# Kernel optimization log

Measured on AMD Instinct MI355X. Metric: run time of the kernel, lower is better.

The kernel has to match this reference:

```python
import math
import jax, jax.numpy as jnp
import numpy as np

B, S, D = 4, 2048, 1024
L = 2                      # codec_decoder_transformer_lengths entry
H, HD = 8, 128             # n_heads == n_kv_heads (no GQA repeat)
FF = 4096
WINDOW = 16                # sliding window (causal: keys in [i-16, i])
NORM_EPS = 0.01
QK_EPS = 1e-6
SCALE_INIT = 0.1           # layer_id < 18 -> 0.1


def _alibi_slopes(n):
    # n is a power of 2 here (8)
    r = 2.0 ** (-8.0 / n)
    return jnp.array([r ** (i + 1) for i in range(n)], dtype=jnp.float32)


def rms_norm(x, w, eps):
    return x * jax.lax.rsqrt(jnp.mean(x * x, axis=-1, keepdims=True) + eps) * w


def _attn_bias(dtype):
    pos = jnp.arange(S)
    rel = pos[None, :] - pos[:, None]          # [S,S], rel = j - i
    slopes = _alibi_slopes(H).astype(dtype)
    bias = slopes[:, None, None] * rel[None].astype(dtype)   # [H,S,S]
    mask = (rel > 0) | (rel < -WINDOW)         # causal + sliding window
    return jnp.where(mask[None], -jnp.inf, bias)


def setup_inputs() -> dict:
    key = jax.random.key(0)
    ks = jax.random.split(key, 9)
    sd = 0.02
    w = lambda k, shape: jax.random.normal(k, shape, jnp.float32) * sd
    return {
        "x": jax.random.normal(ks[0], (B, S, D), jnp.float32),
        "wq": w(ks[1], (L, D, H * HD)),
        "wk": w(ks[2], (L, D, H * HD)),
        "wv": w(ks[3], (L, D, H * HD)),
        "wo": w(ks[4], (L, H * HD, D)),
        "q_norm_w": jnp.ones((L, H * HD), jnp.float32),
        "k_norm_w": jnp.ones((L, H * HD), jnp.float32),
        "w1": w(ks[5], (L, D, FF)),
        "w2": w(ks[6], (L, FF, D)),
        "w3": w(ks[7], (L, D, FF)),
        "attn_norm_w": jnp.ones((L, D), jnp.float32),
        "ffn_norm_w": jnp.ones((L, D), jnp.float32),
        "attn_scale": jnp.full((L, D), SCALE_INIT, jnp.float32),
        "ffn_scale": jnp.full((L, D), SCALE_INIT, jnp.float32),
    }


def reference(x, wq, wk, wv, wo, q_norm_w, k_norm_w, w1, w2, w3,
              attn_norm_w, ffn_norm_w, attn_scale, ffn_scale):
    bias = _attn_bias(x.dtype)                 # [H,S,S]
    inv_sqrt_d = 1.0 / math.sqrt(HD)

    def block(h, p):
        (lwq, lwk, lwv, lwo, qnw, knw, lw1, lw2, lw3, anw, fnw, asc, fsc) = p
        xn = rms_norm(h, anw, NORM_EPS)
        # qk_norm applied on the flat (H*HD) projection before the head split
        q = rms_norm(xn @ lwq, qnw, QK_EPS).reshape(B, S, H, HD).transpose(0, 2, 1, 3)
        k = rms_norm(xn @ lwk, knw, QK_EPS).reshape(B, S, H, HD).transpose(0, 2, 1, 3)
        v = (xn @ lwv).reshape(B, S, H, HD).transpose(0, 2, 1, 3)
        scores = jnp.einsum('bhqd,bhkd->bhqk', q, k) * inv_sqrt_d + bias[None]
        attn = jax.nn.softmax(scores, axis=-1)
        y = jnp.einsum('bhqk,bhkd->bhqd', attn, v)
        y = y.transpose(0, 2, 1, 3).reshape(B, S, H * HD)
        h = h + asc * (y @ lwo)
        xn = rms_norm(h, fnw, NORM_EPS)
        ff = (jax.nn.silu(xn @ lw1) * (xn @ lw3)) @ lw2
        return h + fsc * ff, None

    out, _ = jax.lax.scan(
        block, x,
        (wq, wk, wv, wo, q_norm_w, k_norm_w, w1, w2, w3,
         attn_norm_w, ffn_norm_w, attn_scale, ffn_scale))
    return out
```

## Files before the change

### kernel.cpp

```cpp
#include <hip/hip_runtime.h>

#define B_ 4
#define S_ 2048
#define D_ 1024
#define H_ 8
#define HD_ 128
#define FF_ 4096
#define R_ (B_*S_)

typedef __attribute__((ext_vector_type(8))) short short8;
typedef __attribute__((ext_vector_type(4))) float f32x4;

__device__ __forceinline__ unsigned short f2bf(float f) {
  unsigned int u = __float_as_uint(f);
  return (unsigned short)((u + 0x7fffu + ((u >> 16) & 1u)) >> 16);
}
__device__ __forceinline__ float bf2f(unsigned short s) {
  return __uint_as_float(((unsigned int)s) << 16);
}

typedef const __attribute__((address_space(1))) unsigned int* gas_p;
typedef __attribute__((address_space(3))) unsigned int* las_p;
__device__ __forceinline__ void gload16(const void* g, void* l) {
  __builtin_amdgcn_global_load_lds((gas_p)g, (las_p)l, 16, 0, 0);
}

__global__ __launch_bounds__(256) void f2bf_t_all(
    const float* __restrict__ wq, const float* __restrict__ wk,
    const float* __restrict__ wv, const float* __restrict__ wo,
    const float* __restrict__ w1, const float* __restrict__ w3,
    const float* __restrict__ w2,
    unsigned short* __restrict__ qkvt, unsigned short* __restrict__ wot,
    unsigned short* __restrict__ w1t, unsigned short* __restrict__ w3t,
    unsigned short* __restrict__ w2t) {
  const int id = blockIdx.x;
  const int l = id >> 14, r = id & 16383;
  const float* src; unsigned short* dst; int Rows, Cols, t2;
  if (r < 4096) {
    Rows = 1024; Cols = 1024; t2 = r & 1023;
    const int wsel = r >> 10;
    if (wsel == 0)      { src = wq + (size_t)l*1048576u; dst = qkvt + (size_t)l*3145728u; }
    else if (wsel == 1) { src = wk + (size_t)l*1048576u; dst = qkvt + (size_t)l*3145728u + 1048576u; }
    else if (wsel == 2) { src = wv + (size_t)l*1048576u; dst = qkvt + (size_t)l*3145728u + 2097152u; }
    else                { src = wo + (size_t)l*1048576u; dst = wot + (size_t)l*1048576u; }
  } else if (r < 12288) {
    Rows = 1024; Cols = 4096; t2 = (r - 4096) & 4095;
    if (r < 8192) { src = w1 + (size_t)l*4194304u; dst = w1t + (size_t)l*4194304u; }
    else          { src = w3 + (size_t)l*4194304u; dst = w3t + (size_t)l*4194304u; }
  } else {
    Rows = 4096; Cols = 1024; t2 = r - 12288;
    src = w2 + (size_t)l*4194304u; dst = w2t + (size_t)l*4194304u;
  }
  const int lgc = (Cols == 4096) ? 7 : 5;
  const int bx = t2 & ((1 << lgc) - 1), by = t2 >> lgc;
  const int r0 = by * 32, c0 = bx * 32;
  __shared__ float tile[32][33];
  const int tx = threadIdx.x & 31, ty = threadIdx.x >> 5;
  #pragma unroll
  for (int j = 0; j < 32; j += 8)
    tile[ty + j][tx] = src[(size_t)(r0 + ty + j) * Cols + c0 + tx];
  __syncthreads();
  #pragma unroll
  for (int j = 0; j < 32; j += 8)
    dst[(size_t)(c0 + ty + j) * Rows + r0 + tx] = f2bf(tile[tx][ty + j]);
}

__global__ __launch_bounds__(256) void rmsnorm_f2b(const float* __restrict__ in,
    const float* __restrict__ w, unsigned short* __restrict__ out, float eps) {
  const int row = blockIdx.x, t = threadIdx.x;
  const float4 xv = *(const float4*)&in[(size_t)row * D_ + t * 4];
  float p = xv.x*xv.x + xv.y*xv.y + xv.z*xv.z + xv.w*xv.w;
  #pragma unroll
  for (int off = 32; off >= 1; off >>= 1) p += __shfl_xor(p, off);
  __shared__ float red[4];
  if ((t & 63) == 0) red[t >> 6] = p;
  __syncthreads();
  float scl = rsqrtf((red[0] + red[1] + red[2] + red[3]) * (1.0f / D_) + eps);
  const float4 wv = *(const float4*)&w[t * 4];
  ((ushort4*)out)[(size_t)row * 256 + t] = make_ushort4(
      f2bf(xv.x*scl*wv.x), f2bf(xv.y*scl*wv.y), f2bf(xv.z*scl*wv.z), f2bf(xv.w*scl*wv.w));
}

__global__ __launch_bounds__(256) void qknorm_k(unsigned short* __restrict__ qkv,
    const float* __restrict__ qw, const float* __restrict__ kw) {
  const int row = blockIdx.x, t = threadIdx.x;
  unsigned short* qp = qkv + (size_t)row * 3072;
  unsigned short* kp = qp + 1024;
  const ushort4 qv = ((const ushort4*)qp)[t];
  const ushort4 kv = ((const ushort4*)kp)[t];
  float q0 = bf2f(qv.x), q1 = bf2f(qv.y), q2 = bf2f(qv.z), q3 = bf2f(qv.w);
  float k0 = bf2f(kv.x), k1 = bf2f(kv.y), k2 = bf2f(kv.z), k3 = bf2f(kv.w);
  float pq = q0*q0 + q1*q1 + q2*q2 + q3*q3;
  float pk = k0*k0 + k1*k1 + k2*k2 + k3*k3;
  #pragma unroll
  for (int off = 32; off >= 1; off >>= 1) { pq += __shfl_xor(pq, off); pk += __shfl_xor(pk, off); }
  __shared__ float redq[4], redk[4];
  if ((t & 63) == 0) { redq[t >> 6] = pq; redk[t >> 6] = pk; }
  __syncthreads();
  float sq = rsqrtf((redq[0]+redq[1]+redq[2]+redq[3]) * (1.0f / D_) + 1e-6f);
  float sk = rsqrtf((redk[0]+redk[1]+redk[2]+redk[3]) * (1.0f / D_) + 1e-6f);
  const float4 qwv = *(const float4*)&qw[t * 4];
  const float4 kwv = *(const float4*)&kw[t * 4];
  ((ushort4*)qp)[t] = make_ushort4(f2bf(q0*sq*qwv.x), f2bf(q1*sq*qwv.y),
                                   f2bf(q2*sq*qwv.z), f2bf(q3*sq*qwv.w));
  ((ushort4*)kp)[t] = make_ushort4(f2bf(k0*sk*kwv.x), f2bf(k1*sk*kwv.y),
                                   f2bf(k2*sk*kwv.z), f2bf(k3*sk*kwv.w));
}

__global__ __launch_bounds__(256) void attn_k(const unsigned short* __restrict__ qkv,
    unsigned short* __restrict__ y) {
  const int lane = threadIdx.x & 63;
  const int wid = (blockIdx.x * 256 + threadIdx.x) >> 6;
  const int qq = lane >> 4, li = lane & 15;
  const int grp = wid & (S_/4 - 1);
  const int bh  = wid >> 9;
  const int hh = bh & (H_ - 1);
  const int b  = bh >> 3;
  const int i  = grp * 4 + qq;
  const float slope = exp2f(-(float)(hh + 1));
  const float inv = 0.088388347648318447f;
  const size_t rowq = ((size_t)(b * S_ + i)) * 3072 + hh * HD_ + li * 8;
  const short8 qv8 = *(const short8*)&qkv[rowq];
  float qf[8];
  #pragma unroll
  for (int e = 0; e < 8; ++e) qf[e] = bf2f((unsigned short)qv8[e]);
  float sc[17];
  #pragma unroll
  for (int jj = 0; jj < 17; ++jj) {
    int j = i - 16 + jj;
    int jc = j < 0 ? 0 : j;
    size_t koff = ((size_t)(b * S_ + jc)) * 3072 + 1024 + hh * HD_ + li * 8;
    short8 kv = *(const short8*)&qkv[koff];
    float p = 0.f;
    #pragma unroll
    for (int e = 0; e < 8; ++e) p += qf[e] * bf2f((unsigned short)kv[e]);
    p += __shfl_xor(p, 8); p += __shfl_xor(p, 4);
    p += __shfl_xor(p, 2); p += __shfl_xor(p, 1);
    sc[jj] = (j >= 0) ? (p * inv + slope * (float)(jj - 16)) : -1e30f;
  }
  float m = sc[0];
  #pragma unroll
  for (int jj = 1; jj < 17; ++jj) m = fmaxf(m, sc[jj]);
  float wsum = 0.f, ax[8];
  #pragma unroll
  for (int e = 0; e < 8; ++e) ax[e] = 0.f;
  #pragma unroll
  for (int jj = 0; jj < 17; ++jj) {
    int j = i - 16 + jj;
    int jc = j < 0 ? 0 : j;
    float wgt = expf(sc[jj] - m);
    size_t voff = ((size_t)(b * S_ + jc)) * 3072 + 2048 + hh * HD_ + li * 8;
    short8 vv = *(const short8*)&qkv[voff];
    wsum += wgt;
    #pragma unroll
    for (int e = 0; e < 8; ++e) ax[e] += wgt * bf2f((unsigned short)vv[e]);
  }
  float rs = 1.f / wsum;
  short8 ov;
  #pragma unroll
  for (int e = 0; e < 8; ++e) ov[e] = (short)f2bf(ax[e] * rs);
  size_t yoff = ((size_t)(b * S_ + i)) * 1024 + hh * HD_ + li * 8;
  *(short8*)&y[yoff] = ov;
}

__device__ __forceinline__ void stage_tile(const unsigned short* __restrict__ src,
    unsigned short* lds, int rowbase, int K, int k0, int t) {
  #pragma unroll
  for (int it = 0; it < 4; ++it) {
    int g = it * 256 + t;
    int row = g >> 3, slot = g & 7;
    int sc8 = (slot ^ (row & 7)) << 3;
    gload16(&src[(size_t)(rowbase + row) * K + k0 + sc8], &lds[g * 8]);
  }
}

template<int EPI>
__global__ __launch_bounds__(256, 2) void gemm_tn(
    const unsigned short* __restrict__ A, const unsigned short* __restrict__ Bt,
    void* __restrict__ Cout, const float* __restrict__ sc,
    const float* __restrict__ x2, int M, int N, int K) {
  __shared__ __align__(16) unsigned short As[128 * 64];
  __shared__ __align__(16) unsigned short Bs[128 * 64];
  const int t = threadIdx.x;
  const int lane = t & 63, w = t >> 6;
  const int wr = w >> 1, wc = w & 1;
  const int br = blockIdx.y * 128, bc = blockIdx.x * 128;
  const int lr = lane & 15, lk = lane >> 4;
  const int xm = lr & 7;
  f32x4 acc[4][4];
  #pragma unroll
  for (int mi = 0; mi < 4; ++mi)
    #pragma unroll
    for (int ni = 0; ni < 4; ++ni) { f32x4 z = {0.f,0.f,0.f,0.f}; acc[mi][ni] = z; }
  for (int k0 = 0; k0 < K; k0 += 64) {
    stage_tile(A,  As, br, K, k0, t);
    stage_tile(Bt, Bs, bc, K, k0, t);
    __syncthreads();
    #pragma unroll
    for (int kk = 0; kk < 2; ++kk) {
      short8 af[4], bfr[4];
      #pragma unroll
      for (int mi = 0; mi < 4; ++mi)
        af[mi] = *(const short8*)&As[(wr*64 + mi*16 + lr) * 64 + (((kk*4 + lk) ^ xm) << 3)];
      #pragma unroll
      for (int ni = 0; ni < 4; ++ni)
        bfr[ni] = *(const short8*)&Bs[(wc*64 + ni*16 + lr) * 64 + (((kk*4 + lk) ^ xm) << 3)];
      #pragma unroll
      for (int mi = 0; mi < 4; ++mi)
        #pragma unroll
        for (int ni = 0; ni < 4; ++ni)
          acc[mi][ni] = __builtin_amdgcn_mfma_f32_16x16x32_bf16(af[mi], bfr[ni], acc[mi][ni], 0, 0, 0);
    }
    __syncthreads();
  }
  if (EPI == 0) {
    unsigned short* C = (unsigned short*)Cout;
    #pragma unroll
    for (int mi = 0; mi < 4; ++mi)
      #pragma unroll
      for (int ni = 0; ni < 4; ++ni) {
        int row = br + wr * 64 + mi * 16 + lk * 4;
        int col = bc + wc * 64 + ni * 16 + lr;
        #pragma unroll
        for (int r = 0; r < 4; ++r)
          C[(size_t)(row + r) * N + col] = f2bf(acc[mi][ni][r]);
      }
  } else if (EPI == 1) {
    float* hp = (float*)Cout;
    #pragma unroll
    for (int ni = 0; ni < 4; ++ni) {
      int col = bc + wc * 64 + ni * 16 + lr;
      float sv = sc[col];
      #pragma unroll
      for (int mi = 0; mi < 4; ++mi) {
        int row = br + wr * 64 + mi * 16 + lk * 4;
        #pragma unroll
        for (int r = 0; r < 4; ++r)
          hp[(size_t)(row + r) * N + col] += sv * acc[mi][ni][r];
      }
    }
  } else {
    float* hp = (float*)Cout;
    #pragma unroll
    for (int ni = 0; ni < 4; ++ni) {
      int col = bc + wc * 64 + ni * 16 + lr;
      float sv = sc[col];
      #pragma unroll
      for (int mi = 0; mi < 4; ++mi) {
        int row = br + wr * 64 + mi * 16 + lk * 4;
        #pragma unroll
        for (int r = 0; r < 4; ++r)
          hp[(size_t)(row + r) * N + col] = x2[(size_t)(row + r) * N + col] + sv * acc[mi][ni][r];
      }
    }
  }
}

template<int EPI>
__global__ __launch_bounds__(512, 1) void gemm_dp(
    const unsigned short* __restrict__ A, const unsigned short* __restrict__ Bt,
    float* __restrict__ hp, const float* __restrict__ sc,
    const float* __restrict__ x2, int M, int N, int K) {
  __shared__ __align__(16) unsigned short lds[3][24576];
  const int t = threadIdx.x;
  const int lane = t & 63, w = t >> 6;
  const int wm = w >> 2, wn = w & 3;
  const int lr = lane & 15, lk = lane >> 4;
  const int xm = lr & 7;
  const int br = blockIdx.y << 8, bc = blockIdx.x << 7;

  const unsigned short* Ab = A + (size_t)br * K;
  const unsigned short* Bb = Bt + (size_t)bc * K;

  auto stage = [&](int buf, int k0) {
    unsigned short* d = lds[buf];
    #pragma unroll
    for (int j = 0; j < 4; ++j) {
      int idx = t + (j << 9);
      int row = idx >> 3, slot = idx & 7;
      gload16(Ab + (size_t)row * K + k0 + ((slot ^ (row & 7)) << 3),
              &d[row * 64 + slot * 8]);
    }
    #pragma unroll
    for (int j = 0; j < 2; ++j) {
      int idx = t + (j << 9);
      int row = idx >> 3, slot = idx & 7;
      gload16(Bb + (size_t)row * K + k0 + ((slot ^ (row & 7)) << 3),
              &d[16384 + row * 64 + slot * 8]);
    }
  };

  f32x4 acc[8][2];
  #pragma unroll
  for (int mi = 0; mi < 8; ++mi)
    #pragma unroll
    for (int ni = 0; ni < 2; ++ni) { f32x4 z = {0.f,0.f,0.f,0.f}; acc[mi][ni] = z; }

  const int NT = K >> 6;
  stage(0, 0); stage(1, 64);
  asm volatile("s_waitcnt vmcnt(6)" ::: "memory");
  __builtin_amdgcn_s_barrier();

  #pragma unroll 1
  for (int kt = 0; kt < NT; ++kt) {
    const unsigned short* cur = lds[kt % 3];
    short8 af[2][8], bfr[2][2];
    #pragma unroll
    for (int ks = 0; ks < 2; ++ks) {
      #pragma unroll
      for (int mf = 0; mf < 8; ++mf)
        af[ks][mf] = *(const short8*)&cur[(wm*128 + mf*16 + lr)*64 + (((ks*4+lk)^xm)<<3)];
      #pragma unroll
      for (int nf = 0; nf < 2; ++nf)
        bfr[ks][nf] = *(const short8*)&cur[16384 + (wn*32 + nf*16 + lr)*64 + (((ks*4+lk)^xm)<<3)];
    }
    const int kp = (kt + 2 < NT) ? ((kt + 2) << 6) : 0;
    stage((kt + 2) % 3, kp);
    asm volatile("s_waitcnt vmcnt(6)" ::: "memory");
    asm volatile("s_waitcnt lgkmcnt(0)" ::: "memory");
    __builtin_amdgcn_sched_barrier(0);
    __builtin_amdgcn_s_barrier();
    __builtin_amdgcn_s_setprio(1);
    #pragma unroll
    for (int mf = 0; mf < 8; ++mf)
      #pragma unroll
      for (int nf = 0; nf < 2; ++nf)
        #pragma unroll
        for (int ks = 0; ks < 2; ++ks)
          acc[mf][nf] = __builtin_amdgcn_mfma_f32_16x16x32_bf16(af[ks][mf], bfr[ks][nf], acc[mf][nf], 0, 0, 0);
    __builtin_amdgcn_s_setprio(0);
  }

  #pragma unroll
  for (int nf = 0; nf < 2; ++nf) {
    int col = bc + wn*32 + nf*16 + lr;
    float sv = sc[col];
    #pragma unroll
    for (int mf = 0; mf < 8; ++mf) {
      int row = br + wm*128 + mf*16 + lk*4;
      #pragma unroll
      for (int r = 0; r < 4; ++r) {
        if (EPI == 1)
          hp[(size_t)(row + r) * N + col] += sv * acc[mf][nf][r];
        else
          hp[(size_t)(row + r) * N + col] = x2[(size_t)(row + r) * N + col] + sv * acc[mf][nf][r];
      }
    }
  }
}

__global__ __launch_bounds__(256, 2) void gemm_w13(
    const unsigned short* __restrict__ A, const unsigned short* __restrict__ B1t,
    const unsigned short* __restrict__ B3t, unsigned short* __restrict__ G,
    int M, int N, int K) {
  __shared__ __align__(16) unsigned short As[128 * 64];
  __shared__ __align__(16) unsigned short B1s[128 * 64];
  __shared__ __align__(16) unsigned short B3s[128 * 64];
  const int t = threadIdx.x;
  const int lane = t & 63, w = t >> 6;
  const int wr = w >> 1, wc = w & 1;
  const int br = blockIdx.y * 128, bc = blockIdx.x * 128;
  const int lr = lane & 15, lk = lane >> 4;
  const int xm = lr & 7;
  f32x4 acc1[4][4], acc3[4][4];
  #pragma unroll
  for (int mi = 0; mi < 4; ++mi)
    #pragma unroll
    for (int ni = 0; ni < 4; ++ni) {
      f32x4 z = {0.f,0.f,0.f,0.f}; acc1[mi][ni] = z; acc3[mi][ni] = z;
    }
  for (int k0 = 0; k0 < K; k0 += 64) {
    stage_tile(A,   As,  br, K, k0, t);
    stage_tile(B1t, B1s, bc, K, k0, t);
    stage_tile(B3t, B3s, bc, K, k0, t);
    __syncthreads();
    #pragma unroll
    for (int kk = 0; kk < 2; ++kk) {
      short8 af[4], b1r[4], b3r[4];
      #pragma unroll
      for (int mi = 0; mi < 4; ++mi)
        af[mi] = *(const short8*)&As[(wr*64 + mi*16 + lr) * 64 + (((kk*4 + lk) ^ xm) << 3)];
      #pragma unroll
      for (int ni = 0; ni < 4; ++ni) {
        b1r[ni] = *(const short8*)&B1s[(wc*64 + ni*16 + lr) * 64 + (((kk*4 + lk) ^ xm) << 3)];
        b3r[ni] = *(const short8*)&B3s[(wc*64 + ni*16 + lr) * 64 + (((kk*4 + lk) ^ xm) << 3)];
      }
      #pragma unroll
      for (int mi = 0; mi < 4; ++mi)
        #pragma unroll
        for (int ni = 0; ni < 4; ++ni) {
          acc1[mi][ni] = __builtin_amdgcn_mfma_f32_16x16x32_bf16(af[mi], b1r[ni], acc1[mi][ni], 0, 0, 0);
          acc3[mi][ni] = __builtin_amdgcn_mfma_f32_16x16x32_bf16(af[mi], b3r[ni], acc3[mi][ni], 0, 0, 0);
        }
    }
    __syncthreads();
  }
  #pragma unroll
  for (int mi = 0; mi < 4; ++mi)
    #pragma unroll
    for (int ni = 0; ni < 4; ++ni) {
      int row = br + wr * 64 + mi * 16 + lk * 4;
      int col = bc + wc * 64 + ni * 16 + lr;
      #pragma unroll
      for (int r = 0; r < 4; ++r) {
        float a1 = acc1[mi][ni][r], a3 = acc3[mi][ni][r];
        G[(size_t)(row + r) * N + col] = f2bf(a1 / (1.f + expf(-a1)) * a3);
      }
    }
}

extern "C" void kernel_launch(void* const* d_in, const int* in_sizes, int n_in,
                              void* d_out, int out_size, void* d_ws, size_t ws_size,
                              hipStream_t stream) {
  const float* x    = (const float*)d_in[0];
  const float* wq   = (const float*)d_in[1];
  const float* wk   = (const float*)d_in[2];
  const float* wv   = (const float*)d_in[3];
  const float* wo   = (const float*)d_in[4];
  const float* qnw  = (const float*)d_in[5];
  const float* knw  = (const float*)d_in[6];
  const float* w1   = (const float*)d_in[7];
  const float* w2   = (const float*)d_in[8];
  const float* w3   = (const float*)d_in[9];
  const float* anw  = (const float*)d_in[10];
  const float* fnw  = (const float*)d_in[11];
  const float* asc  = (const float*)d_in[12];
  const float* fsc  = (const float*)d_in[13];

  const size_t MB = 1024 * 1024;
  if (ws_size < 144 * MB) return;

  float* h = (float*)d_out;
  char* ws = (char*)d_ws;
  unsigned short* qkvt = (unsigned short*)ws;
  unsigned short* wot  = qkvt + 2u * 3145728u;
  unsigned short* w1t  = wot  + 2u * 1048576u;
  unsigned short* w3t  = w1t  + 2u * 4194304u;
  unsigned short* w2t  = w3t  + 2u * 4194304u;
  unsigned short* xn   = (unsigned short*)(ws + 64 * MB);
  unsigned short* qkv  = (unsigned short*)(ws + 80 * MB);
  unsigned short* gate = qkv;

  f2bf_t_all<<<32768, 256, 0, stream>>>(wq, wk, wv, wo, w1, w3, w2,
                                        qkvt, wot, w1t, w3t, w2t);

  for (int l = 0; l < 2; ++l) {
    rmsnorm_f2b<<<R_, 256, 0, stream>>>(l == 0 ? x : h, anw + l * D_, xn, 0.01f);
    gemm_tn<0><<<dim3(24, 64), 256, 0, stream>>>(xn, qkvt + (size_t)l*3145728u, qkv,
                                                 nullptr, nullptr, R_, 3072, 1024);
    qknorm_k<<<R_, 256, 0, stream>>>(qkv, qnw + l * 1024, knw + l * 1024);
    attn_k<<<R_ * H_ / 16, 256, 0, stream>>>(qkv, xn);
    if (l == 0)
      gemm_dp<2><<<dim3(8, 32), 512, 0, stream>>>(xn, wot, h, asc, x, R_, 1024, 1024);
    else
      gemm_dp<1><<<dim3(8, 32), 512, 0, stream>>>(xn, wot + 1048576u, h, asc + D_,
                                                  nullptr, R_, 1024, 1024);
    rmsnorm_f2b<<<R_, 256, 0, stream>>>(h, fnw + l * D_, xn, 0.01f);
    gemm_w13<<<dim3(32, 64), 256, 0, stream>>>(xn, w1t + (size_t)l*4194304u,
                                               w3t + (size_t)l*4194304u, gate, R_, 4096, 1024);
    gemm_dp<1><<<dim3(8, 32), 512, 0, stream>>>(gate, w2t + (size_t)l*4194304u, h,
                                                fsc + l * D_, nullptr, R_, 1024, 4096);
  }
}
```

Before: 823.0 us.

## Route QKV and W1/W3 GEMMs through the pipelined gemm_dp kernel with interleaved weights

Removes the simple gemm_tn and gemm_w13 kernels. The QKV projection and the SwiGLU gate GEMM now run on the larger, triple-buffered gemm_dp kernel, which gains bf16-store and fused SiLU-gate epilogues. To feed the gate epilogue, W1 and W3 are interleaved in 16-column groups during the one-time weight transpose, so each warp holds matching w1/w3 fragments and the gate GEMM becomes a single N=8192 GEMM. The aim is better MFMA utilisation and latency hiding from the pipelined kernel. The cost is a bigger tile that may underfill the GPU or raise register pressure.

```diff
diff --git a/kernel.cpp b/kernel.cpp
--- a/kernel.cpp
+++ b/kernel.cpp
@@ -31,11 +31,11 @@
     const float* __restrict__ w1, const float* __restrict__ w3,
     const float* __restrict__ w2,
     unsigned short* __restrict__ qkvt, unsigned short* __restrict__ wot,
-    unsigned short* __restrict__ w1t, unsigned short* __restrict__ w3t,
-    unsigned short* __restrict__ w2t) {
+    unsigned short* __restrict__ w13t, unsigned short* __restrict__ w2t) {
   const int id = blockIdx.x;
   const int l = id >> 14, r = id & 16383;
   const float* src; unsigned short* dst; int Rows, Cols, t2;
+  bool inter = false, sel3 = false;
   if (r < 4096) {
     Rows = 1024; Cols = 1024; t2 = r & 1023;
     const int wsel = r >> 10;
@@ -45,8 +45,9 @@
     else                { src = wo + (size_t)l*1048576u; dst = wot + (size_t)l*1048576u; }
   } else if (r < 12288) {
     Rows = 1024; Cols = 4096; t2 = (r - 4096) & 4095;
-    if (r < 8192) { src = w1 + (size_t)l*4194304u; dst = w1t + (size_t)l*4194304u; }
-    else          { src = w3 + (size_t)l*4194304u; dst = w3t + (size_t)l*4194304u; }
+    inter = true; sel3 = (r >= 8192);
+    src = (sel3 ? w3 : w1) + (size_t)l*4194304u;
+    dst = w13t + (size_t)l*8388608u;
   } else {
     Rows = 4096; Cols = 1024; t2 = r - 12288;
     src = w2 + (size_t)l*4194304u; dst = w2t + (size_t)l*4194304u;
@@ -61,8 +62,11 @@
     tile[ty + j][tx] = src[(size_t)(r0 + ty + j) * Cols + c0 + tx];
   __syncthreads();
   #pragma unroll
-  for (int j = 0; j < 32; j += 8)
-    dst[(size_t)(c0 + ty + j) * Rows + r0 + tx] = f2bf(tile[tx][ty + j]);
+  for (int j = 0; j < 32; j += 8) {
+    int c = c0 + ty + j;
+    int drow = inter ? (((c >> 4) << 5) + (sel3 ? 16 : 0) + (c & 15)) : c;
+    dst[(size_t)drow * Rows + r0 + tx] = f2bf(tile[tx][ty + j]);
+  }
 }
 
 __global__ __launch_bounds__(256) void rmsnorm_f2b(const float* __restrict__ in,
@@ -163,103 +167,10 @@
   *(short8*)&y[yoff] = ov;
 }
 
-__device__ __forceinline__ void stage_tile(const unsigned short* __restrict__ src,
-    unsigned short* lds, int rowbase, int K, int k0, int t) {
-  #pragma unroll
-  for (int it = 0; it < 4; ++it) {
-    int g = it * 256 + t;
-    int row = g >> 3, slot = g & 7;
-    int sc8 = (slot ^ (row & 7)) << 3;
-    gload16(&src[(size_t)(rowbase + row) * K + k0 + sc8], &lds[g * 8]);
-  }
-}
-
-template<int EPI>
-__global__ __launch_bounds__(256, 2) void gemm_tn(
-    const unsigned short* __restrict__ A, const unsigned short* __restrict__ Bt,
-    void* __restrict__ Cout, const float* __restrict__ sc,
-    const float* __restrict__ x2, int M, int N, int K) {
-  __shared__ __align__(16) unsigned short As[128 * 64];
-  __shared__ __align__(16) unsigned short Bs[128 * 64];
-  const int t = threadIdx.x;
-  const int lane = t & 63, w = t >> 6;
-  const int wr = w >> 1, wc = w & 1;
-  const int br = blockIdx.y * 128, bc = blockIdx.x * 128;
-  const int lr = lane & 15, lk = lane >> 4;
-  const int xm = lr & 7;
-  f32x4 acc[4][4];
-  #pragma unroll
-  for (int mi = 0; mi < 4; ++mi)
-    #pragma unroll
-    for (int ni = 0; ni < 4; ++ni) { f32x4 z = {0.f,0.f,0.f,0.f}; acc[mi][ni] = z; }
-  for (int k0 = 0; k0 < K; k0 += 64) {
-    stage_tile(A,  As, br, K, k0, t);
-    stage_tile(Bt, Bs, bc, K, k0, t);
-    __syncthreads();
-    #pragma unroll
-    for (int kk = 0; kk < 2; ++kk) {
-      short8 af[4], bfr[4];
-      #pragma unroll
-      for (int mi = 0; mi < 4; ++mi)
-        af[mi] = *(const short8*)&As[(wr*64 + mi*16 + lr) * 64 + (((kk*4 + lk) ^ xm) << 3)];
-      #pragma unroll
-      for (int ni = 0; ni < 4; ++ni)
-        bfr[ni] = *(const short8*)&Bs[(wc*64 + ni*16 + lr) * 64 + (((kk*4 + lk) ^ xm) << 3)];
-      #pragma unroll
-      for (int mi = 0; mi < 4; ++mi)
-        #pragma unroll
-        for (int ni = 0; ni < 4; ++ni)
-          acc[mi][ni] = __builtin_amdgcn_mfma_f32_16x16x32_bf16(af[mi], bfr[ni], acc[mi][ni], 0, 0, 0);
-    }
-    __syncthreads();
-  }
-  if (EPI == 0) {
-    unsigned short* C = (unsigned short*)Cout;
-    #pragma unroll
-    for (int mi = 0; mi < 4; ++mi)
-      #pragma unroll
-      for (int ni = 0; ni < 4; ++ni) {
-        int row = br + wr * 64 + mi * 16 + lk * 4;
-        int col = bc + wc * 64 + ni * 16 + lr;
-        #pragma unroll
-        for (int r = 0; r < 4; ++r)
-          C[(size_t)(row + r) * N + col] = f2bf(acc[mi][ni][r]);
-      }
-  } else if (EPI == 1) {
-    float* hp = (float*)Cout;
-    #pragma unroll
-    for (int ni = 0; ni < 4; ++ni) {
-      int col = bc + wc * 64 + ni * 16 + lr;
-      float sv = sc[col];
-      #pragma unroll
-      for (int mi = 0; mi < 4; ++mi) {
-        int row = br + wr * 64 + mi * 16 + lk * 4;
-        #pragma unroll
-        for (int r = 0; r < 4; ++r)
-          hp[(size_t)(row + r) * N + col] += sv * acc[mi][ni][r];
-      }
-    }
-  } else {
-    float* hp = (float*)Cout;
-    #pragma unroll
-    for (int ni = 0; ni < 4; ++ni) {
-      int col = bc + wc * 64 + ni * 16 + lr;
-      float sv = sc[col];
-      #pragma unroll
-      for (int mi = 0; mi < 4; ++mi) {
-        int row = br + wr * 64 + mi * 16 + lk * 4;
-        #pragma unroll
-        for (int r = 0; r < 4; ++r)
-          hp[(size_t)(row + r) * N + col] = x2[(size_t)(row + r) * N + col] + sv * acc[mi][ni][r];
-      }
-    }
-  }
-}
-
 template<int EPI>
 __global__ __launch_bounds__(512, 1) void gemm_dp(
     const unsigned short* __restrict__ A, const unsigned short* __restrict__ Bt,
-    float* __restrict__ hp, const float* __restrict__ sc,
+    void* __restrict__ Cout, const float* __restrict__ sc,
     const float* __restrict__ x2, int M, int N, int K) {
   __shared__ __align__(16) unsigned short lds[3][24576];
   const int t = threadIdx.x;
@@ -331,82 +242,50 @@
     __builtin_amdgcn_s_setprio(0);
   }
 
-  #pragma unroll
-  for (int nf = 0; nf < 2; ++nf) {
-    int col = bc + wn*32 + nf*16 + lr;
-    float sv = sc[col];
+  if (EPI == 0) {
+    unsigned short* C = (unsigned short*)Cout;
+    #pragma unroll
+    for (int mf = 0; mf < 8; ++mf)
+      #pragma unroll
+      for (int nf = 0; nf < 2; ++nf) {
+        int row = br + wm*128 + mf*16 + lk*4;
+        int col = bc + wn*32 + nf*16 + lr;
+        #pragma unroll
+        for (int r = 0; r < 4; ++r)
+          C[(size_t)(row + r) * N + col] = f2bf(acc[mf][nf][r]);
+      }
+  } else if (EPI == 3) {
+    unsigned short* G = (unsigned short*)Cout;
+    const int NG = N >> 1;
+    int gcol = (bc >> 1) + wn*16 + lr;
     #pragma unroll
     for (int mf = 0; mf < 8; ++mf) {
       int row = br + wm*128 + mf*16 + lk*4;
       #pragma unroll
       for (int r = 0; r < 4; ++r) {
-        if (EPI == 1)
-          hp[(size_t)(row + r) * N + col] += sv * acc[mf][nf][r];
-        else
-          hp[(size_t)(row + r) * N + col] = x2[(size_t)(row + r) * N + col] + sv * acc[mf][nf][r];
+        float a1 = acc[mf][0][r], a3 = acc[mf][1][r];
+        G[(size_t)(row + r) * NG + gcol] = f2bf(a1 / (1.f + expf(-a1)) * a3);
       }
     }
-  }
-}
-
-__global__ __launch_bounds__(256, 2) void gemm_w13(
-    const unsigned short* __restrict__ A, const unsigned short* __restrict__ B1t,
-    const unsigned short* __restrict__ B3t, unsigned short* __restrict__ G,
-    int M, int N, int K) {
-  __shared__ __align__(16) unsigned short As[128 * 64];
-  __shared__ __align__(16) unsigned short B1s[128 * 64];
-  __shared__ __align__(16) unsigned short B3s[128 * 64];
-  const int t = threadIdx.x;
-  const int lane = t & 63, w = t >> 6;
-  const int wr = w >> 1, wc = w & 1;
-  const int br = blockIdx.y * 128, bc = blockIdx.x * 128;
-  const int lr = lane & 15, lk = lane >> 4;
-  const int xm = lr & 7;
-  f32x4 acc1[4][4], acc3[4][4];
-  #pragma unroll
-  for (int mi = 0; mi < 4; ++mi)
-    #pragma unroll
-    for (int ni = 0; ni < 4; ++ni) {
-      f32x4 z = {0.f,0.f,0.f,0.f}; acc1[mi][ni] = z; acc3[mi][ni] = z;
-    }
-  for (int k0 = 0; k0 < K; k0 += 64) {
-    stage_tile(A,   As,  br, K, k0, t);
-    stage_tile(B1t, B1s, bc, K, k0, t);
-    stage_tile(B3t, B3s, bc, K, k0, t);
-    __syncthreads();
-    #pragma unroll
-    for (int kk = 0; kk < 2; ++kk) {
-      short8 af[4], b1r[4], b3r[4];
-      #pragma unroll
-      for (int mi = 0; mi < 4; ++mi)
-        af[mi] = *(const short8*)&As[(wr*64 + mi*16 + lr) * 64 + (((kk*4 + lk) ^ xm) << 3)];
-      #pragma unroll
-      for (int ni = 0; ni < 4; ++ni) {
-        b1r[ni] = *(const short8*)&B1s[(wc*64 + ni*16 + lr) * 64 + (((kk*4 + lk) ^ xm) << 3)];
-        b3r[ni] = *(const short8*)&B3s[(wc*64 + ni*16 + lr) * 64 + (((kk*4 + lk) ^ xm) << 3)];
+  } else {
+    float* hp = (float*)Cout;
+    #pragma unroll
+    for (int nf = 0; nf < 2; ++nf) {
+      int col = bc + wn*32 + nf*16 + lr;
+      float sv = sc[col];
+      #pragma unroll
+      for (int mf = 0; mf < 8; ++mf) {
+        int row = br + wm*128 + mf*16 + lk*4;
+        #pragma unroll
+        for (int r = 0; r < 4; ++r) {
+          if (EPI == 1)
+            hp[(size_t)(row + r) * N + col] += sv * acc[mf][nf][r];
+          else
+            hp[(size_t)(row + r) * N + col] = x2[(size_t)(row + r) * N + col] + sv * acc[mf][nf][r];
+        }
       }
-      #pragma unroll
-      for (int mi = 0; mi < 4; ++mi)
-        #pragma unroll
-        for (int ni = 0; ni < 4; ++ni) {
-          acc1[mi][ni] = __builtin_amdgcn_mfma_f32_16x16x32_bf16(af[mi], b1r[ni], acc1[mi][ni], 0, 0, 0);
-          acc3[mi][ni] = __builtin_amdgcn_mfma_f32_16x16x32_bf16(af[mi], b3r[ni], acc3[mi][ni], 0, 0, 0);
-        }
-    }
-    __syncthreads();
-  }
-  #pragma unroll
-  for (int mi = 0; mi < 4; ++mi)
-    #pragma unroll
-    for (int ni = 0; ni < 4; ++ni) {
-      int row = br + wr * 64 + mi * 16 + lk * 4;
-      int col = bc + wc * 64 + ni * 16 + lr;
-      #pragma unroll
-      for (int r = 0; r < 4; ++r) {
-        float a1 = acc1[mi][ni][r], a3 = acc3[mi][ni][r];
-        G[(size_t)(row + r) * N + col] = f2bf(a1 / (1.f + expf(-a1)) * a3);
-      }
-    }
+    }
+  }
 }
 
 extern "C" void kernel_launch(void* const* d_in, const int* in_sizes, int n_in,
@@ -434,19 +313,18 @@
   char* ws = (char*)d_ws;
   unsigned short* qkvt = (unsigned short*)ws;
   unsigned short* wot  = qkvt + 2u * 3145728u;
-  unsigned short* w1t  = wot  + 2u * 1048576u;
-  unsigned short* w3t  = w1t  + 2u * 4194304u;
-  unsigned short* w2t  = w3t  + 2u * 4194304u;
+  unsigned short* w13t = wot  + 2u * 1048576u;
+  unsigned short* w2t  = w13t + 2u * 8388608u;
   unsigned short* xn   = (unsigned short*)(ws + 64 * MB);
   unsigned short* qkv  = (unsigned short*)(ws + 80 * MB);
   unsigned short* gate = qkv;
 
   f2bf_t_all<<<32768, 256, 0, stream>>>(wq, wk, wv, wo, w1, w3, w2,
-                                        qkvt, wot, w1t, w3t, w2t);
+                                        qkvt, wot, w13t, w2t);
 
   for (int l = 0; l < 2; ++l) {
     rmsnorm_f2b<<<R_, 256, 0, stream>>>(l == 0 ? x : h, anw + l * D_, xn, 0.01f);
-    gemm_tn<0><<<dim3(24, 64), 256, 0, stream>>>(xn, qkvt + (size_t)l*3145728u, qkv,
+    gemm_dp<0><<<dim3(24, 32), 512, 0, stream>>>(xn, qkvt + (size_t)l*3145728u, qkv,
                                                  nullptr, nullptr, R_, 3072, 1024);
     qknorm_k<<<R_, 256, 0, stream>>>(qkv, qnw + l * 1024, knw + l * 1024);
     attn_k<<<R_ * H_ / 16, 256, 0, stream>>>(qkv, xn);
@@ -456,8 +334,8 @@
       gemm_dp<1><<<dim3(8, 32), 512, 0, stream>>>(xn, wot + 1048576u, h, asc + D_,
                                                   nullptr, R_, 1024, 1024);
     rmsnorm_f2b<<<R_, 256, 0, stream>>>(h, fnw + l * D_, xn, 0.01f);
-    gemm_w13<<<dim3(32, 64), 256, 0, stream>>>(xn, w1t + (size_t)l*4194304u,
-                                               w3t + (size_t)l*4194304u, gate, R_, 4096, 1024);
+    gemm_dp<3><<<dim3(64, 32), 512, 0, stream>>>(xn, w13t + (size_t)l*8388608u, gate,
+                                                 nullptr, nullptr, R_, 8192, 1024);
     gemm_dp<1><<<dim3(8, 32), 512, 0, stream>>>(gate, w2t + (size_t)l*4194304u, h,
                                                 fsc + l * D_, nullptr, R_, 1024, 4096);
   }
```

After: 898.5 us. 1.09x slower.

## Triple-buffer the fused W1/W3 gate GEMM with async LDS prefetch

Applied to the files above, without the earlier changes.

Replaces the single-buffered W1/W3 gate GEMM with a triple-buffered version. The A, B1 and B3 tiles are staged directly into LDS with global_load_lds two K-tiles ahead, and each iteration synchronises only once, using explicit waitcnt, a barrier and raised priority around the MFMA block. The aim is to overlap global loads with matrix math and drop one barrier per K step. The cost is 144KB of LDS per block, so occupancy falls to one block per CU (launch bounds lowered to 1), and the vmcnt accounting is hand-tuned and fragile.

```diff
diff --git a/kernel.cpp b/kernel.cpp
--- a/kernel.cpp
+++ b/kernel.cpp
@@ -349,19 +349,47 @@
   }
 }
 
-__global__ __launch_bounds__(256, 2) void gemm_w13(
+__global__ __launch_bounds__(256, 1) void gemm_w13_dp(
     const unsigned short* __restrict__ A, const unsigned short* __restrict__ B1t,
     const unsigned short* __restrict__ B3t, unsigned short* __restrict__ G,
     int M, int N, int K) {
-  __shared__ __align__(16) unsigned short As[128 * 64];
-  __shared__ __align__(16) unsigned short B1s[128 * 64];
-  __shared__ __align__(16) unsigned short B3s[128 * 64];
+  __shared__ __align__(16) unsigned short lds[3][24576];
   const int t = threadIdx.x;
   const int lane = t & 63, w = t >> 6;
   const int wr = w >> 1, wc = w & 1;
   const int br = blockIdx.y * 128, bc = blockIdx.x * 128;
   const int lr = lane & 15, lk = lane >> 4;
   const int xm = lr & 7;
+
+  const unsigned short* Ab  = A   + (size_t)br * K;
+  const unsigned short* B1b = B1t + (size_t)bc * K;
+  const unsigned short* B3b = B3t + (size_t)bc * K;
+
+  auto stage = [&](int buf, int k0) {
+    unsigned short* d = lds[buf];
+    #pragma unroll
+    for (int it = 0; it < 4; ++it) {
+      int g = it * 256 + t;
+      int row = g >> 3, slot = g & 7;
+      int sc8 = (slot ^ (row & 7)) << 3;
+      gload16(Ab  + (size_t)row * K + k0 + sc8, &d[g * 8]);
+    }
+    #pragma unroll
+    for (int it = 0; it < 4; ++it) {
+      int g = it * 256 + t;
+      int row = g >> 3, slot = g & 7;
+      int sc8 = (slot ^ (row & 7)) << 3;
+      gload16(B1b + (size_t)row * K + k0 + sc8, &d[8192 + g * 8]);
+    }
+    #pragma unroll
+    for (int it = 0; it < 4; ++it) {
+      int g = it * 256 + t;
+      int row = g >> 3, slot = g & 7;
+      int sc8 = (slot ^ (row & 7)) << 3;
+      gload16(B3b + (size_t)row * K + k0 + sc8, &d[16384 + g * 8]);
+    }
+  };
+
   f32x4 acc1[4][4], acc3[4][4];
   #pragma unroll
   for (int mi = 0; mi < 4; ++mi)
@@ -369,32 +397,44 @@
     for (int ni = 0; ni < 4; ++ni) {
       f32x4 z = {0.f,0.f,0.f,0.f}; acc1[mi][ni] = z; acc3[mi][ni] = z;
     }
-  for (int k0 = 0; k0 < K; k0 += 64) {
-    stage_tile(A,   As,  br, K, k0, t);
-    stage_tile(B1t, B1s, bc, K, k0, t);
-    stage_tile(B3t, B3s, bc, K, k0, t);
-    __syncthreads();
-    #pragma unroll
-    for (int kk = 0; kk < 2; ++kk) {
-      short8 af[4], b1r[4], b3r[4];
-      #pragma unroll
-      for (int mi = 0; mi < 4; ++mi)
-        af[mi] = *(const short8*)&As[(wr*64 + mi*16 + lr) * 64 + (((kk*4 + lk) ^ xm) << 3)];
-      #pragma unroll
-      for (int ni = 0; ni < 4; ++ni) {
-        b1r[ni] = *(const short8*)&B1s[(wc*64 + ni*16 + lr) * 64 + (((kk*4 + lk) ^ xm) << 3)];
-        b3r[ni] = *(const short8*)&B3s[(wc*64 + ni*16 + lr) * 64 + (((kk*4 + lk) ^ xm) << 3)];
+
+  const int NT = K >> 6;
+  stage(0, 0); stage(1, 64);
+  asm volatile("s_waitcnt vmcnt(12)" ::: "memory");
+  __builtin_amdgcn_s_barrier();
+
+  #pragma unroll 1
+  for (int kt = 0; kt < NT; ++kt) {
+    const unsigned short* cur = lds[kt % 3];
+    short8 af[2][4], b1r[2][4], b3r[2][4];
+    #pragma unroll
+    for (int kk = 0; kk < 2; ++kk)
+      #pragma unroll
+      for (int mi = 0; mi < 4; ++mi) {
+        int off = (((kk*4 + lk) ^ xm) << 3);
+        af[kk][mi]  = *(const short8*)&cur[(wr*64 + mi*16 + lr) * 64 + off];
+        b1r[kk][mi] = *(const short8*)&cur[8192  + (wc*64 + mi*16 + lr) * 64 + off];
+        b3r[kk][mi] = *(const short8*)&cur[16384 + (wc*64 + mi*16 + lr) * 64 + off];
       }
+    const int kp = (kt + 2 < NT) ? ((kt + 2) << 6) : 0;
+    stage((kt + 2) % 3, kp);
+    asm volatile("s_waitcnt vmcnt(12)" ::: "memory");
+    asm volatile("s_waitcnt lgkmcnt(0)" ::: "memory");
+    __builtin_amdgcn_sched_barrier(0);
+    __builtin_amdgcn_s_barrier();
+    __builtin_amdgcn_s_setprio(1);
+    #pragma unroll
+    for (int kk = 0; kk < 2; ++kk)
       #pragma unroll
       for (int mi = 0; mi < 4; ++mi)
         #pragma unroll
         for (int ni = 0; ni < 4; ++ni) {
-          acc1[mi][ni] = __builtin_amdgcn_mfma_f32_16x16x32_bf16(af[mi], b1r[ni], acc1[mi][ni], 0, 0, 0);
-          acc3[mi][ni] = __builtin_amdgcn_mfma_f32_16x16x32_bf16(af[mi], b3r[ni], acc3[mi][ni], 0, 0, 0);
+          acc1[mi][ni] = __builtin_amdgcn_mfma_f32_16x16x32_bf16(af[kk][mi], b1r[kk][ni], acc1[mi][ni], 0, 0, 0);
+          acc3[mi][ni] = __builtin_amdgcn_mfma_f32_16x16x32_bf16(af[kk][mi], b3r[kk][ni], acc3[mi][ni], 0, 0, 0);
         }
-    }
-    __syncthreads();
-  }
+    __builtin_amdgcn_s_setprio(0);
+  }
+
   #pragma unroll
   for (int mi = 0; mi < 4; ++mi)
     #pragma unroll
@@ -456,8 +496,8 @@
       gemm_dp<1><<<dim3(8, 32), 512, 0, stream>>>(xn, wot + 1048576u, h, asc + D_,
                                                   nullptr, R_, 1024, 1024);
     rmsnorm_f2b<<<R_, 256, 0, stream>>>(h, fnw + l * D_, xn, 0.01f);
-    gemm_w13<<<dim3(32, 64), 256, 0, stream>>>(xn, w1t + (size_t)l*4194304u,
-                                               w3t + (size_t)l*4194304u, gate, R_, 4096, 1024);
+    gemm_w13_dp<<<dim3(32, 64), 256, 0, stream>>>(xn, w1t + (size_t)l*4194304u,
+                                                  w3t + (size_t)l*4194304u, gate, R_, 4096, 1024);
     gemm_dp<1><<<dim3(8, 32), 512, 0, stream>>>(gate, w2t + (size_t)l*4194304u, h,
                                                 fsc + l * D_, nullptr, R_, 1024, 4096);
   }
```

New measurement: 995.6 us. 21.0% more time.
